# Kernel tuning notes

Hardware: AMD Instinct MI355X
Metric: run time of the kernel (lower is better)

Reference implementation:

```python
import jax, jax.numpy as jnp
from jax import lax
import numpy as np

# static config (matches init_kwargs)
B, H, Wd, C = 32, 96, 96, 64
nW, K, PAD = 4, 3, 1
WS = 48  # window_size = H // sqrt(nW)


def setup_inputs() -> dict:
    key = jax.random.key(0)
    ks = jax.random.split(key, 24)
    def p(i, shape, s=0.02):
        return jax.random.normal(ks[i], shape, dtype=jnp.float32) * s
    return {
        "x": jax.random.normal(ks[0], (B, H * Wd, C), dtype=jnp.float32),
        # se: conv1x1 -> gelu -> conv1x1 -> sigmoid
        "se_w1": p(1, (C, C)), "se_b1": p(2, (C,)),
        "se_w2": p(3, (C, C)), "se_b2": p(4, (C,)),
        # WinKernel_Reweight
        "dc_w": p(5, (nW, C)), "dc_b": p(6, (nW,)),            # grouped 1x1, nW groups of C->1
        "l1_w": p(7, (4 * nW, nW)), "l1_b": p(8, (4 * nW,)),
        "l2_w": p(9, (nW, 4 * nW)), "l2_b": p(10, (nW,)),
        # gk_fusion: grouped 1x1 (dim groups, nW->1 per group)
        "gkf_w": p(11, (C, nW)), "gkf_b": p(12, (C,)),
        # Fusion (gk_sum)
        "fu_proj_w": p(13, (C, nW, nW)), "fu_proj_b": p(14, (C * nW,)),  # grouped 1x1, dim groups of nW->nW
        "fu_fc1_w": p(15, (C, nW * C)), "fu_fc1_b": p(16, (C,)),
        "fu_fc2_w": p(17, (nW * C, C)), "fu_fc2_b": p(18, (nW * C,)),
        "fu_po_w": p(19, (C, C)), "fu_po_b": p(20, (C,)),
        # final proj_out
        "po_w": p(21, (C, C)), "po_b": p(22, (C,)),
    }


def _gelu(t):
    return jax.nn.gelu(t, approximate=False)  # torch nn.GELU default = exact erf


def _conv1x1(w, b, t):
    return jnp.einsum('oi,bihw->bohw', w, t) + b[None, :, None, None]


def _forward(x, se_w1, se_b1, se_w2, se_b2, dc_w, dc_b, l1_w, l1_b, l2_w, l2_b,
             gkf_w, gkf_b, fu_proj_w, fu_proj_b, fu_fc1_w, fu_fc1_b,
             fu_fc2_w, fu_fc2_b, fu_po_w, fu_po_b, po_w, po_b):
    xh = x.reshape(B, H, Wd, C)
    # window_partition -> (B*nW, C, WS, WS), windows row-major within each batch element
    win = (xh.reshape(B, 2, WS, 2, WS, C)
             .transpose(0, 1, 3, 2, 4, 5)
             .reshape(B * nW, WS, WS, C)
             .transpose(0, 3, 1, 2))
    # adaptive avg pool (WS->K, exact since WS % K == 0)
    pool = WS // K
    kern = win.reshape(B * nW, C, K, pool, K, pool).mean(axis=(3, 5))  # (B*nW, C, K, K)
    # SE block replaces kernels
    kern_se = jax.nn.sigmoid(_conv1x1(se_w2, se_b2, _gelu(_conv1x1(se_w1, se_b1, kern))))
    # WinKernel_Reweight
    xwin = win.reshape(B, nW * C, WS, WS)
    ww = xwin.mean(axis=(2, 3)).reshape(B, nW, C)                 # GAP then grouped 1x1 (nW groups)
    ww = jnp.einsum('wc,bwc->bw', dc_w, ww) + dc_b                # (B, nW)
    ww = _gelu(ww @ l1_w.T + l1_b)
    ww = jax.nn.sigmoid(ww @ l2_w.T + l2_b)                       # (B, nW)
    kr = kern_se.reshape(B, nW, C, K, K) * ww[:, :, None, None, None]
    # gk_fusion: after transpose(1,2) channel order is c-major; grouped conv -> per-c mix over windows
    gkf = jnp.einsum('cw,bwcij->bcij', gkf_w, kr) + gkf_b[None, :, None, None]  # (B, C, K, K)
    # Fusion (gk_sum) on SE kernels (window-major channel layout)
    feats_in = kern_se.reshape(B, nW * C, K, K)
    fg = feats_in.reshape(B, C, nW, K, K)                         # groups = consecutive nW channels
    feats = _gelu(jnp.einsum('goi,bgikl->bgokl', fu_proj_w, fg)
                  + fu_proj_b.reshape(1, C, nW, 1, 1))
    v = feats.mean(axis=(3, 4)).reshape(B, C * nW)                # GAP
    v = _gelu(v @ fu_fc1_w.T + fu_fc1_b)                          # (B, C)
    av = jax.nn.softmax((v @ fu_fc2_w.T + fu_fc2_b).reshape(B, nW, C), axis=1)
    x_sum = jnp.einsum('bwckl,bwc->bckl', feats_in.reshape(B, nW, C, K, K), av)
    gks = gkf + _conv1x1(fu_po_w, fu_po_b, x_sum)                 # (B, C, K, K)
    # assemble per-(sample, kernel-branch, channel) depthwise kernels and convolve
    gk = jnp.stack([gkf, gks], axis=1).reshape(B * 2 * C, 1, K, K)
    xi = jnp.broadcast_to(xh.transpose(0, 3, 1, 2)[:, None], (B, 2, C, H, Wd))
    xi = xi.reshape(1, B * 2 * C, H, Wd)
    y = lax.conv_general_dilated(xi, gk, window_strides=(1, 1),
                                 padding=((PAD, PAD), (PAD, PAD)),
                                 feature_group_count=B * 2 * C,
                                 dimension_numbers=('NCHW', 'OIHW', 'NCHW'))
    y = y.reshape(B, 2, C, H, Wd).sum(axis=1)                     # sum the two kernel branches
    y = _conv1x1(po_w, po_b, y)
    return y.transpose(0, 2, 3, 1).reshape(B, H * Wd, C)


def reference(x, se_w1, se_b1, se_w2, se_b2, dc_w, dc_b, l1_w, l1_b, l2_w, l2_b,
              gkf_w, gkf_b, fu_proj_w, fu_proj_b, fu_fc1_w, fu_fc1_b,
              fu_fc2_w, fu_fc2_b, fu_po_w, fu_po_b, po_w, po_b):
    return _forward(x, se_w1, se_b1, se_w2, se_b2, dc_w, dc_b, l1_w, l1_b, l2_w, l2_b,
                    gkf_w, gkf_b, fu_proj_w, fu_proj_b, fu_fc1_w, fu_fc1_b,
                    fu_fc2_w, fu_fc2_b, fu_po_w, fu_po_b, po_w, po_b)
```

## Files before the change

### kernel.cpp

```cpp
#include <hip/hip_runtime.h>
#include <hip/hip_bf16.h>

#define NPIX 9216

typedef __attribute__((ext_vector_type(8))) short short8v;
typedef __attribute__((ext_vector_type(4))) float floatx4;

__device__ __forceinline__ float geluf(float x){
  return 0.5f * x * (1.0f + erff(x * 0.70710678118654752440f));
}
__device__ __forceinline__ float sigm(float x){
  return 1.0f / (1.0f + expf(-x));
}
__device__ __forceinline__ unsigned short f2bf(float f){
  __hip_bfloat16 h = __float2bfloat16(f);
  return *(unsigned short*)&h;
}

__global__ __launch_bounds__(256) void k_pool(const float* __restrict__ x,
                                              const float* __restrict__ po_w,
                                              float* __restrict__ kern,
                                              unsigned short* __restrict__ frag_pw)
{
  int blk = blockIdx.x;
  int t = threadIdx.x;
  if (blk == 0){
    for (int idx=t; idx<4096; idx+=256){
      int f = idx >> 9, L = (idx >> 3) & 63, j = idx & 7;
      int nb = f >> 1, kb = f & 1;
      int o = nb*16 + (L & 15);
      int c = kb*32 + ((L >> 4) & 3)*8 + j;
      frag_pw[idx] = f2bf(po_w[o*64 + c]);
    }
  }
  int bw = blk / 9, rem = blk % 9;
  int ki = rem / 3, kj = rem % 3;
  int b = bw >> 2, w = bw & 3;
  int wr = w >> 1, wc = w & 1;
  int cg = t & 15, rw = t >> 4;
  int h = wr*48 + ki*16 + rw;
  int col0 = wc*48 + kj*16;
  size_t base = ((size_t)(b*NPIX + h*96 + col0))*64 + cg*4;
  float a0=0.f,a1=0.f,a2=0.f,a3=0.f;
  #pragma unroll
  for (int j=0;j<16;j++){
    float4 u = *(const float4*)(x + base + (size_t)j*64);
    a0 += u.x; a1 += u.y; a2 += u.z; a3 += u.w;
  }
  __shared__ float red[16*64];
  float* rr = &red[rw*64 + cg*4];
  rr[0]=a0; rr[1]=a1; rr[2]=a2; rr[3]=a3;
  __syncthreads();
  if (t < 64){
    float s = 0.f;
    #pragma unroll
    for (int r=0;r<16;r++) s += red[r*64 + t];
    kern[(size_t)bw*576 + t*9 + rem] = s * (1.0f/256.0f);
  }
}

__global__ __launch_bounds__(512) void k_fuse(const float* __restrict__ kern_ws,
    const float* __restrict__ se_w1, const float* __restrict__ se_b1,
    const float* __restrict__ se_w2, const float* __restrict__ se_b2,
    const float* __restrict__ dc_w,  const float* __restrict__ dc_b,
    const float* __restrict__ l1_w,  const float* __restrict__ l1_b,
    const float* __restrict__ l2_w,  const float* __restrict__ l2_b,
    const float* __restrict__ gkf_w, const float* __restrict__ gkf_b,
    const float* __restrict__ fu_proj_w, const float* __restrict__ fu_proj_b,
    const float* __restrict__ fu_fc1_w,  const float* __restrict__ fu_fc1_b,
    const float* __restrict__ fu_fc2_w,  const float* __restrict__ fu_fc2_b,
    const float* __restrict__ fu_po_w,   const float* __restrict__ fu_po_b,
    float* __restrict__ kc_ws)
{
  int b = blockIdx.x;
  int t = threadIdx.x;
  int lane = t & 63, wv = t >> 6;

  __shared__ float s_w1[64*65];
  __shared__ float s_w2[64*65];
  __shared__ float s_pow[64*65];
  __shared__ float s_kern[4*64*13];
  __shared__ float s_t1[4*64*13];
  __shared__ float s_kse[2304];
  __shared__ float s_prj[1088];
  __shared__ float s_feats[2304];
  __shared__ float s_gkf[576];
  __shared__ float s_xsum[576];
  __shared__ float s_wwc[256];
  __shared__ float s_v0[256];
  __shared__ float s_av[256];
  __shared__ float s_v1[64];
  __shared__ float s_small[64];

  for (int idx=t; idx<2304; idx+=512){
    int w = idx/576, cp = idx - w*576;
    int c = cp/9, p = cp - c*9;
    s_kern[(w*64+c)*13+p] = kern_ws[(size_t)(b*4+w)*576 + cp];
  }
  for (int j=t; j<4096; j+=512){
    int o=j>>6, i=j&63;
    s_w1[i*65+o]  = se_w1[j];
    s_w2[i*65+o]  = se_w2[j];
    s_pow[i*65+o] = fu_po_w[j];
  }
  for (int j=t; j<1024; j+=512){ int g=j>>4, oi=j&15; s_prj[g*17+oi] = fu_proj_w[j]; }
  __syncthreads();

  for (int idx=t; idx<2304; idx+=512){
    int o = idx & 63, wp = idx >> 6;
    int w = wp/9, p = wp - w*9;
    float acc = se_b1[o];
    #pragma unroll 8
    for (int i=0;i<64;i++) acc += s_w1[i*65+o]*s_kern[(w*64+i)*13+p];
    s_t1[(w*64+o)*13+p] = geluf(acc);
  }
  if (t < 256){
    const float* kr = &s_kern[t*13];
    float s = kr[0]+kr[1]+kr[2]+kr[3]+kr[4]+kr[5]+kr[6]+kr[7]+kr[8];
    s_wwc[t] = s * (1.0f/9.0f);
  }
  __syncthreads();

  for (int idx=t; idx<2304; idx+=512){
    int o = idx & 63, wp = idx >> 6;
    int w = wp/9, p = wp - w*9;
    float acc = se_b2[o];
    #pragma unroll 8
    for (int i=0;i<64;i++) acc += s_w2[i*65+o]*s_t1[(w*64+i)*13+p];
    s_kse[w*576 + o*9 + p] = sigm(acc);
  }
  if (t < 4){
    float acc = dc_b[t];
    #pragma unroll 8
    for (int c=0;c<64;c++) acc += dc_w[t*64+c]*s_wwc[t*64+c];
    s_small[t] = acc;
  }
  __syncthreads();

  for (int idx=t; idx<2304; idx+=512){
    int g = idx & 63, op = idx >> 6;
    int o = op/9, p = op - o*9;
    float acc = fu_proj_b[g*4+o];
    #pragma unroll
    for (int i=0;i<4;i++){
      int ch = g*4+i;
      acc += s_prj[g*17 + o*4 + i] * s_kse[(ch>>6)*576 + (ch&63)*9 + p];
    }
    s_feats[(g*4+o)*9 + p] = geluf(acc);
  }
  if (t < 16){
    float acc = l1_b[t];
    #pragma unroll
    for (int w=0;w<4;w++) acc += l1_w[t*4+w]*s_small[w];
    s_small[16+t] = geluf(acc);
  }
  __syncthreads();

  if (t < 256){
    const float* f = &s_feats[t*9];
    s_v0[t] = (f[0]+f[1]+f[2]+f[3]+f[4]+f[5]+f[6]+f[7]+f[8]) * (1.0f/9.0f);
  } else if (t < 260){
    int tt = t - 256;
    float acc = l2_b[tt];
    #pragma unroll
    for (int j=0;j<16;j++) acc += l2_w[tt*16+j]*s_small[16+j];
    s_small[32+tt] = sigm(acc);
  }
  __syncthreads();

  #pragma unroll
  for (int oi=0; oi<8; oi++){
    int o = wv*8 + oi;
    float v = fu_fc1_w[o*256 +       lane] * s_v0[      lane]
            + fu_fc1_w[o*256 +  64 + lane] * s_v0[ 64 + lane]
            + fu_fc1_w[o*256 + 128 + lane] * s_v0[128 + lane]
            + fu_fc1_w[o*256 + 192 + lane] * s_v0[192 + lane];
    #pragma unroll
    for (int m=32; m>0; m>>=1) v += __shfl_xor(v, m);
    if (lane == 0) s_v1[o] = geluf(v + fu_fc1_b[o]);
  }
  __syncthreads();

  if (t < 256){
    const float4* wr = (const float4*)(fu_fc2_w + t*64);
    float acc = 0.f;
    #pragma unroll
    for (int q=0;q<16;q++){
      float4 wq = wr[q];
      acc += wq.x*s_v1[q*4] + wq.y*s_v1[q*4+1] + wq.z*s_v1[q*4+2] + wq.w*s_v1[q*4+3];
    }
    s_av[t] = acc + fu_fc2_b[t];
  }
  for (int idx=t; idx<576; idx+=512){
    int c = idx & 63, p = idx >> 6;
    float acc = gkf_b[c];
    #pragma unroll
    for (int w=0;w<4;w++) acc += gkf_w[c*4+w]*s_kse[w*576+c*9+p]*s_small[32+w];
    s_gkf[c*9+p] = acc;
  }
  __syncthreads();

  if (t < 64){
    float z0=s_av[t], z1=s_av[64+t], z2=s_av[128+t], z3=s_av[192+t];
    float mx = fmaxf(fmaxf(z0,z1),fmaxf(z2,z3));
    float e0=expf(z0-mx), e1=expf(z1-mx), e2=expf(z2-mx), e3=expf(z3-mx);
    float inv = 1.0f/(e0+e1+e2+e3);
    s_av[t]=e0*inv; s_av[64+t]=e1*inv; s_av[128+t]=e2*inv; s_av[192+t]=e3*inv;
  }
  __syncthreads();

  for (int idx=t; idx<576; idx+=512){
    int c = idx & 63, p = idx >> 6;
    float s=0.f;
    #pragma unroll
    for (int w=0;w<4;w++) s += s_kse[w*576+c*9+p]*s_av[w*64+c];
    s_xsum[c*9+p] = s;
  }
  __syncthreads();

  for (int idx=t; idx<576; idx+=512){
    int c = idx & 63, p = idx >> 6;
    float acc = 2.0f*s_gkf[c*9+p] + fu_po_b[c];
    #pragma unroll 8
    for (int i=0;i<64;i++) acc += s_pow[i*65+c]*s_xsum[i*9+p];
    kc_ws[(size_t)b*576 + c*9 + p] = acc;
  }
}

__global__ __launch_bounds__(256, 5) void k_conv(const float* __restrict__ x,
                                                 const float* __restrict__ kc_ws,
                                                 const unsigned short* __restrict__ frag_pw,
                                                 const float* __restrict__ po_b,
                                                 float* __restrict__ out)
{
  int bi_hw = blockIdx.x;
  int bi = (bi_hw & 7) * 576 + (bi_hw >> 3);
  int b = bi / 144, tile = bi % 144;
  int th = tile / 12, tw = tile % 12;
  int h0 = th*8, w0 = tw*8;
  int t = threadIdx.x;
  int c = t & 63, rg = t >> 6;
  int r0 = rg*2;

  __shared__ __align__(16) float s_buf[4352];
  unsigned short* s_tmp = (unsigned short*)s_buf;
  float* s_out = s_buf;

  const float* kcb = kc_ws + b*576 + c*9;
  float k0=kcb[0],k1=kcb[1],k2=kcb[2],k3=kcb[3],k4=kcb[4],
        k5=kcb[5],k6=kcb[6],k7=kcb[7],k8=kcb[8];

  float row[4][10];
  if (th > 0 && th < 11 && tw > 0 && tw < 11){
    const float* xb = x + (((size_t)(b*NPIX + (h0-1+r0)*96 + (w0-1)))<<6) + c;
    #pragma unroll
    for (int rr=0; rr<4; rr++)
      #pragma unroll
      for (int cc=0; cc<10; cc++)
        row[rr][cc] = xb[((size_t)(rr*96 + cc))<<6];
  } else {
    #pragma unroll
    for (int rr=0; rr<4; rr++){
      int hh = h0 - 1 + r0 + rr;
      bool hok = (hh >= 0 && hh < 96);
      #pragma unroll
      for (int cc=0; cc<10; cc++){
        int ww = w0 - 1 + cc;
        float v = 0.f;
        if (hok && ww >= 0 && ww < 96)
          v = x[(((size_t)b*NPIX + hh*96 + ww)<<6) + c];
        row[rr][cc] = v;
      }
    }
  }

  #pragma unroll
  for (int dr=0; dr<2; dr++){
    int pr = r0 + dr;
    #pragma unroll
    for (int pc=0; pc<8; pc++){
      float acc = k0*row[dr+0][pc] + k1*row[dr+0][pc+1] + k2*row[dr+0][pc+2]
                + k3*row[dr+1][pc] + k4*row[dr+1][pc+1] + k5*row[dr+1][pc+2]
                + k6*row[dr+2][pc] + k7*row[dr+2][pc+1] + k8*row[dr+2][pc+2];
      s_tmp[(pr*8 + pc)*72 + c] = f2bf(acc);
    }
  }
  __syncthreads();

  int wv = t >> 6, lane = t & 63;
  int quad = lane >> 4;
  floatx4 acc[4] = {{0.f,0.f,0.f,0.f},{0.f,0.f,0.f,0.f},
                    {0.f,0.f,0.f,0.f},{0.f,0.f,0.f,0.f}};
  {
    int m = wv*16 + (lane & 15);
    #pragma unroll
    for (int kb=0; kb<2; kb++){
      short8v afrag = *(const short8v*)&s_tmp[m*72 + kb*32 + quad*8];
      #pragma unroll
      for (int nb=0; nb<4; nb++){
        short8v bfrag = *(const short8v*)(frag_pw + (nb*2+kb)*512 + lane*8);
        acc[nb] = __builtin_amdgcn_mfma_f32_16x16x32_bf16(afrag, bfrag, acc[nb], 0, 0, 0);
      }
    }
  }
  __syncthreads();

  {
    #pragma unroll
    for (int nb=0; nb<4; nb++){
      int o = nb*16 + (lane & 15);
      float pb = po_b[o];
      #pragma unroll
      for (int r=0; r<4; r++){
        int px = wv*16 + quad*4 + r;
        s_out[px*68 + o] = acc[nb][r] + pb;
      }
    }
  }
  __syncthreads();

  for (int idx=t; idx<1024; idx+=256){
    int px = idx >> 4, c4 = idx & 15;
    int hh = h0 + (px >> 3), wwp = w0 + (px & 7);
    floatx4 v = *(const floatx4*)&s_out[px*68 + c4*4];
    __builtin_nontemporal_store(v,
        (floatx4*)(out + (((size_t)b*NPIX + hh*96 + wwp)<<6) + c4*4));
  }
}

extern "C" void kernel_launch(void* const* d_in, const int* in_sizes, int n_in,
                              void* d_out, int out_size, void* d_ws, size_t ws_size,
                              hipStream_t stream) {
  const float* x        = (const float*)d_in[0];
  const float* se_w1    = (const float*)d_in[1];
  const float* se_b1    = (const float*)d_in[2];
  const float* se_w2    = (const float*)d_in[3];
  const float* se_b2    = (const float*)d_in[4];
  const float* dc_w     = (const float*)d_in[5];
  const float* dc_b     = (const float*)d_in[6];
  const float* l1_w     = (const float*)d_in[7];
  const float* l1_b     = (const float*)d_in[8];
  const float* l2_w     = (const float*)d_in[9];
  const float* l2_b     = (const float*)d_in[10];
  const float* gkf_w    = (const float*)d_in[11];
  const float* gkf_b    = (const float*)d_in[12];
  const float* fu_proj_w= (const float*)d_in[13];
  const float* fu_proj_b= (const float*)d_in[14];
  const float* fu_fc1_w = (const float*)d_in[15];
  const float* fu_fc1_b = (const float*)d_in[16];
  const float* fu_fc2_w = (const float*)d_in[17];
  const float* fu_fc2_b = (const float*)d_in[18];
  const float* fu_po_w  = (const float*)d_in[19];
  const float* fu_po_b  = (const float*)d_in[20];
  const float* po_w     = (const float*)d_in[21];
  const float* po_b     = (const float*)d_in[22];

  float* kern_ws = (float*)d_ws;
  float* kc_ws   = kern_ws + 73728;
  unsigned short* frag_pw = (unsigned short*)(kc_ws + 18432);

  k_pool<<<1152, 256, 0, stream>>>(x, po_w, kern_ws, frag_pw);
  k_fuse<<<32, 512, 0, stream>>>(kern_ws,
                                 se_w1, se_b1, se_w2, se_b2,
                                 dc_w, dc_b, l1_w, l1_b, l2_w, l2_b,
                                 gkf_w, gkf_b, fu_proj_w, fu_proj_b,
                                 fu_fc1_w, fu_fc1_b, fu_fc2_w, fu_fc2_b,
                                 fu_po_w, fu_po_b, kc_ws);
  k_conv<<<4608, 256, 0, stream>>>(x, kc_ws, frag_pw, po_b, (float*)d_out);
}
```

Baseline: 211.9 us.

## Widen conv tile to 8x16 pixels to cut halo reloads

The depthwise-conv + projection kernel now handles 8x16 pixel tiles per block instead of 8x8, halving the block count. Each thread loads an 18-wide row strip, so the halo overhead per output falls (10/8 to 18/16 columns), and each wave issues two M-tiles of MFMA against the same B fragments. Output is staged through shared memory in two halves so the LDS footprint stays small. The cost is more registers per thread (occupancy hint lowered from 5 to 4 blocks) and an extra barrier round for the split write-out.

```diff
diff --git a/kernel.cpp b/kernel.cpp
--- a/kernel.cpp
+++ b/kernel.cpp
@@ -227,22 +227,22 @@
   }
 }
 
-__global__ __launch_bounds__(256, 5) void k_conv(const float* __restrict__ x,
+__global__ __launch_bounds__(256, 4) void k_conv(const float* __restrict__ x,
                                                  const float* __restrict__ kc_ws,
                                                  const unsigned short* __restrict__ frag_pw,
                                                  const float* __restrict__ po_b,
                                                  float* __restrict__ out)
 {
   int bi_hw = blockIdx.x;
-  int bi = (bi_hw & 7) * 576 + (bi_hw >> 3);
-  int b = bi / 144, tile = bi % 144;
-  int th = tile / 12, tw = tile % 12;
-  int h0 = th*8, w0 = tw*8;
+  int bi = (bi_hw & 7) * 288 + (bi_hw >> 3);
+  int b = bi / 72, tile = bi % 72;
+  int th = tile / 6, tw = tile % 6;
+  int h0 = th*8, w0 = tw*16;
   int t = threadIdx.x;
   int c = t & 63, rg = t >> 6;
   int r0 = rg*2;
 
-  __shared__ __align__(16) float s_buf[4352];
+  __shared__ __align__(16) float s_buf[4608];
   unsigned short* s_tmp = (unsigned short*)s_buf;
   float* s_out = s_buf;
 
@@ -250,13 +250,13 @@
   float k0=kcb[0],k1=kcb[1],k2=kcb[2],k3=kcb[3],k4=kcb[4],
         k5=kcb[5],k6=kcb[6],k7=kcb[7],k8=kcb[8];
 
-  float row[4][10];
-  if (th > 0 && th < 11 && tw > 0 && tw < 11){
+  float row[4][18];
+  if (th > 0 && th < 11 && tw > 0 && tw < 5){
     const float* xb = x + (((size_t)(b*NPIX + (h0-1+r0)*96 + (w0-1)))<<6) + c;
     #pragma unroll
     for (int rr=0; rr<4; rr++)
       #pragma unroll
-      for (int cc=0; cc<10; cc++)
+      for (int cc=0; cc<18; cc++)
         row[rr][cc] = xb[((size_t)(rr*96 + cc))<<6];
   } else {
     #pragma unroll
@@ -264,7 +264,7 @@
       int hh = h0 - 1 + r0 + rr;
       bool hok = (hh >= 0 && hh < 96);
       #pragma unroll
-      for (int cc=0; cc<10; cc++){
+      for (int cc=0; cc<18; cc++){
         int ww = w0 - 1 + cc;
         float v = 0.f;
         if (hok && ww >= 0 && ww < 96)
@@ -278,53 +278,65 @@
   for (int dr=0; dr<2; dr++){
     int pr = r0 + dr;
     #pragma unroll
-    for (int pc=0; pc<8; pc++){
+    for (int pc=0; pc<16; pc++){
       float acc = k0*row[dr+0][pc] + k1*row[dr+0][pc+1] + k2*row[dr+0][pc+2]
                 + k3*row[dr+1][pc] + k4*row[dr+1][pc+1] + k5*row[dr+1][pc+2]
                 + k6*row[dr+2][pc] + k7*row[dr+2][pc+1] + k8*row[dr+2][pc+2];
-      s_tmp[(pr*8 + pc)*72 + c] = f2bf(acc);
+      s_tmp[(pr*16 + pc)*72 + c] = f2bf(acc);
     }
   }
   __syncthreads();
 
   int wv = t >> 6, lane = t & 63;
   int quad = lane >> 4;
-  floatx4 acc[4] = {{0.f,0.f,0.f,0.f},{0.f,0.f,0.f,0.f},
-                    {0.f,0.f,0.f,0.f},{0.f,0.f,0.f,0.f}};
+  floatx4 acc[2][4] = {{{0.f,0.f,0.f,0.f},{0.f,0.f,0.f,0.f},
+                        {0.f,0.f,0.f,0.f},{0.f,0.f,0.f,0.f}},
+                       {{0.f,0.f,0.f,0.f},{0.f,0.f,0.f,0.f},
+                        {0.f,0.f,0.f,0.f},{0.f,0.f,0.f,0.f}}};
   {
-    int m = wv*16 + (lane & 15);
-    #pragma unroll
-    for (int kb=0; kb<2; kb++){
-      short8v afrag = *(const short8v*)&s_tmp[m*72 + kb*32 + quad*8];
+    int m0 = wv*32 + (lane & 15);
+    #pragma unroll
+    for (int mt=0; mt<2; mt++){
       #pragma unroll
-      for (int nb=0; nb<4; nb++){
-        short8v bfrag = *(const short8v*)(frag_pw + (nb*2+kb)*512 + lane*8);
-        acc[nb] = __builtin_amdgcn_mfma_f32_16x16x32_bf16(afrag, bfrag, acc[nb], 0, 0, 0);
+      for (int kb=0; kb<2; kb++){
+        short8v afrag = *(const short8v*)&s_tmp[(m0 + mt*16)*72 + kb*32 + quad*8];
+        #pragma unroll
+        for (int nb=0; nb<4; nb++){
+          short8v bfrag = *(const short8v*)(frag_pw + (nb*2+kb)*512 + lane*8);
+          acc[mt][nb] = __builtin_amdgcn_mfma_f32_16x16x32_bf16(afrag, bfrag, acc[mt][nb], 0, 0, 0);
+        }
       }
     }
   }
   __syncthreads();
 
-  {
-    #pragma unroll
-    for (int nb=0; nb<4; nb++){
-      int o = nb*16 + (lane & 15);
-      float pb = po_b[o];
+  #pragma unroll
+  for (int h=0; h<2; h++){
+    if ((wv >> 1) == h){
       #pragma unroll
-      for (int r=0; r<4; r++){
-        int px = wv*16 + quad*4 + r;
-        s_out[px*68 + o] = acc[nb][r] + pb;
+      for (int mt=0; mt<2; mt++){
+        #pragma unroll
+        for (int nb=0; nb<4; nb++){
+          int o = nb*16 + (lane & 15);
+          float pb = po_b[o];
+          #pragma unroll
+          for (int r=0; r<4; r++){
+            int pxl = (wv & 1)*32 + mt*16 + quad*4 + r;
+            s_out[pxl*68 + o] = acc[mt][nb][r] + pb;
+          }
+        }
       }
     }
-  }
-  __syncthreads();
-
-  for (int idx=t; idx<1024; idx+=256){
-    int px = idx >> 4, c4 = idx & 15;
-    int hh = h0 + (px >> 3), wwp = w0 + (px & 7);
-    floatx4 v = *(const floatx4*)&s_out[px*68 + c4*4];
-    __builtin_nontemporal_store(v,
-        (floatx4*)(out + (((size_t)b*NPIX + hh*96 + wwp)<<6) + c4*4));
+    __syncthreads();
+    for (int idx=t; idx<1024; idx+=256){
+      int pxl = idx >> 4, c4 = idx & 15;
+      int px = h*64 + pxl;
+      int hh = h0 + (px >> 4), wwp = w0 + (px & 15);
+      floatx4 v = *(const floatx4*)&s_out[pxl*68 + c4*4];
+      __builtin_nontemporal_store(v,
+          (floatx4*)(out + (((size_t)b*NPIX + hh*96 + wwp)<<6) + c4*4));
+    }
+    if (h == 0) __syncthreads();
   }
 }
 
@@ -366,5 +378,5 @@
                                  gkf_w, gkf_b, fu_proj_w, fu_proj_b,
                                  fu_fc1_w, fu_fc1_b, fu_fc2_w, fu_fc2_b,
                                  fu_po_w, fu_po_b, kc_ws);
-  k_conv<<<4608, 256, 0, stream>>>(x, kc_ws, frag_pw, po_b, (float*)d_out);
-}
+  k_conv<<<2304, 256, 0, stream>>>(x, kc_ws, frag_pw, po_b, (float*)d_out);
+}
```

Measured after the change: 215.3 us. About the same (+1.6%).
